# Optimization experiments

Hardware: AMD Instinct MI355X
Metric: run time of the kernel (lower is better)

Reference implementation:

```python
import jax, jax.numpy as jnp
import numpy as np

EPS = 1e-5

def _bn(x, g, b, m, v):
    # eval-mode batchnorm, NCHW, per-channel params
    inv = g / jnp.sqrt(v + EPS)
    return x * inv[None, :, None, None] + (b - m * inv)[None, :, None, None]

def setup_inputs() -> dict:
    key = jax.random.key(0)
    ks = jax.random.split(key, 16)
    C = 64
    x = jax.random.normal(ks[0], (8, C, 64, 64), dtype=jnp.float32)
    w1 = jax.random.normal(ks[1], (C, C, 1, 1), dtype=jnp.float32) * 0.1
    w2 = jax.random.normal(ks[2], (C, 1, 3, 3), dtype=jnp.float32) * 0.1
    w3 = jax.random.normal(ks[3], (C, C, 1, 1), dtype=jnp.float32) * 0.1
    def bn_params(k):
        k1, k2, k3, k4 = jax.random.split(k, 4)
        return (jax.random.uniform(k1, (C,)) + 0.5,
                jax.random.normal(k2, (C,)) * 0.1,
                jax.random.normal(k3, (C,)) * 0.1,
                jax.random.uniform(k4, (C,)) + 0.5)
    g1, b1, m1, v1 = bn_params(ks[4])
    g2, b2, m2, v2 = bn_params(ks[5])
    g3, b3, m3, v3 = bn_params(ks[6])
    return {"x": x, "w1": w1, "bn1_g": g1, "bn1_b": b1, "bn1_m": m1, "bn1_v": v1,
            "w2": w2, "bn2_g": g2, "bn2_b": b2, "bn2_m": m2, "bn2_v": v2,
            "w3": w3, "bn3_g": g3, "bn3_b": b3, "bn3_m": m3, "bn3_v": v3}

def reference(x, w1, bn1_g, bn1_b, bn1_m, bn1_v,
              w2, bn2_g, bn2_b, bn2_m, bn2_v,
              w3, bn3_g, bn3_b, bn3_m, bn3_v):
    B, c, h, w = x.shape
    N = h * w
    # conv1 (1x1) + BN + ReLU -> V
    v = jnp.einsum('bchw,oc->bohw', x, w1[:, :, 0, 0])
    v = jax.nn.relu(_bn(v, bn1_g, bn1_b, bn1_m, bn1_v))
    # attention over spatial positions: Q=K=x, single head, dim=c
    Q = x.reshape(B, c, N)          # bdn
    V = v.reshape(B, c, N)          # bdm
    scores = jnp.einsum('bdn,bdm->bnm', Q, Q) / (c ** 0.5)  # [B,N,N]
    prob = jax.nn.softmax(scores, axis=-1)
    out = jnp.einsum('bnm,bdm->bdn', prob, V).reshape(B, c, h, w)
    # depthwise conv + BN + ReLU
    out = jax.lax.conv_general_dilated(
        out, w2, window_strides=(1, 1), padding='SAME',
        dimension_numbers=('NCHW', 'OIHW', 'NCHW'), feature_group_count=c)
    out = jax.nn.relu(_bn(out, bn2_g, bn2_b, bn2_m, bn2_v))
    # pointwise conv + BN
    out = jnp.einsum('bchw,oc->bohw', out, w3[:, :, 0, 0])
    out = _bn(out, bn3_g, bn3_b, bn3_m, bn3_v)
    # residual (stride==1 and in_size==out_size)
    return out + x
```

## Files before the change

kernel.cpp:

```cpp
#include <hip/hip_runtime.h>
#include <stdint.h>

typedef __attribute__((ext_vector_type(8)))  short s16x8;
typedef __attribute__((ext_vector_type(16))) float f32x16;
typedef __attribute__((ext_vector_type(2)))  unsigned u32x2;

union CvtI4 { int4 i; s16x8 s; };
union CvtU4 { uint4 u; s16x8 s; };

__device__ __forceinline__ unsigned f2bf(float f) {
    union { float f; unsigned u; } v; v.f = f;
    return (v.u + 0x7fffu + ((v.u >> 16) & 1u)) >> 16;
}

__device__ __forceinline__ unsigned packbf(float lo, float hi) {
    union { float f; unsigned u; } a0, a1;
    a0.f = lo; a1.f = hi;
    return __builtin_amdgcn_perm(a1.u + 0x8000u, a0.u + 0x8000u, 0x07060302u);
}

__device__ __forceinline__ void gload_lds16(const unsigned short* gsrc, unsigned short* ldst) {
    __builtin_amdgcn_global_load_lds(
        (const __attribute__((address_space(1))) void*)gsrc,
        (__attribute__((address_space(3))) void*)ldst, 16, 0, 0);
}

__global__ __launch_bounds__(256) void k_prep(
    const float* __restrict__ x, const float* __restrict__ w1,
    const float* __restrict__ g1, const float* __restrict__ b1,
    const float* __restrict__ m1, const float* __restrict__ v1,
    unsigned short* __restrict__ xT, unsigned short* __restrict__ vbf)
{
    __shared__ float X[64 * 65];
    const int b    = blockIdx.x >> 7;
    const int n0   = ((blockIdx.x >> 1) & 63) << 6;
    const int half = blockIdx.x & 1;
    const int tid  = threadIdx.x;
    const float QS = 0.42466090014400953f;

    {
        const int r = tid >> 6, nn = tid & 63;
        const float* xb = x + (size_t)b * 262144 + n0 + nn;
#pragma unroll
        for (int cc = 0; cc < 16; ++cc) {
            int c = cc * 4 + r;
            X[c * 65 + nn] = xb[(size_t)c * 4096];
        }
    }
    __syncthreads();

    {
        const int n8 = tid >> 3, c8 = tid & 7;
        const int n = (half << 5) + n8;
        unsigned u[4];
#pragma unroll
        for (int j = 0; j < 4; ++j) {
            unsigned lo = f2bf(X[(c8 * 8 + 2 * j) * 65 + n] * QS);
            unsigned hi = f2bf(X[(c8 * 8 + 2 * j + 1) * 65 + n] * QS);
            u[j] = lo | (hi << 16);
        }
        uint4 pk; pk.x = u[0]; pk.y = u[1]; pk.z = u[2]; pk.w = u[3];
        *(uint4*)(xT + (((size_t)((b << 12) + n0 + n)) << 6) + (c8 << 3)) = pk;
    }

    {
        const int n = tid & 63, og = tid >> 6;
        float rX[64];
#pragma unroll
        for (int c = 0; c < 64; ++c) rX[c] = X[c * 65 + n];
        unsigned short* vb = vbf + (((size_t)(b << 6)) << 12) + n0 + n;
#pragma unroll 2
        for (int oo = 0; oo < 8; ++oo) {
            int o = (half << 5) + og * 8 + oo;
            float inv = g1[o] * rsqrtf(v1[o] + 1e-5f);
            float sh  = b1[o] - m1[o] * inv;
            float acc = 0.f;
#pragma unroll
            for (int c = 0; c < 64; ++c) acc = fmaf(w1[o * 64 + c], rX[c], acc);
            vb[(size_t)o << 12] = (unsigned short)f2bf(fmaxf(fmaf(acc, inv, sh), 0.f));
        }
    }
}

__global__ __launch_bounds__(1024, 4) void k_attn(
    const unsigned short* __restrict__ xT, const unsigned short* __restrict__ vbf,
    unsigned short* __restrict__ outO)
{
    __shared__ __align__(16) unsigned short Kl[2][2][64 * 64];
    __shared__ __align__(16) unsigned short Vl[2][2][64 * 64];
    __shared__ float rsL[16][32];
    __shared__ float dnm[128];

    const int b   = blockIdx.x & 7;
    const int qg2 = blockIdx.x >> 3;
    const int tid = threadIdx.x;
    const int w = tid >> 6, lane = tid & 63;
    const int l31 = lane & 31, half = lane >> 5;
    const int qbase = qg2 << 7;
    const int qd = w & 7, par = w >> 3;
    const int s  = qd & 1;
    const int t2 = qd >> 1;

    s16x8 Bq[4];
    {
        const unsigned short* qr = xT +
            (((size_t)((b << 12) + qbase + (t2 << 5) + l31)) << 6) + (half << 3);
#pragma unroll
        for (int kk = 0; kk < 4; ++kk) {
            CvtI4 c; c.i = *(const int4*)(qr + (kk << 4));
            Bq[kk] = c.s;
        }
    }

    const int pt    = w >> 3;
    const int sr    = ((w & 7) << 3) + (lane >> 3);
    const int swsc  = (lane & 7) ^ (lane >> 3);
    const unsigned short* kSrc = xT  + ((size_t)b << 18) + (sr << 6) + (swsc << 3);
    const unsigned short* vSrc = vbf + ((size_t)b << 18) + ((size_t)sr << 12) + (swsc << 3);
    const int ldsOff = (w & 7) << 9;

    gload_lds16(kSrc + ((size_t)pt << 12), &Kl[0][pt][0] + ldsOff);
    gload_lds16(vSrc + (pt << 6),          &Vl[0][pt][0] + ldsOff);
    __syncthreads();

    f32x16 O[2];
#pragma unroll
    for (int dl = 0; dl < 2; ++dl)
#pragma unroll
        for (int r = 0; r < 16; ++r) O[dl][r] = 0.f;
    float rs = 0.f;

    uint2 Gh[4];
    s16x8 Bvh[4];
    {
        const s16x8 z = {0, 0, 0, 0, 0, 0, 0, 0};
#pragma unroll
        for (int q = 0; q < 4; ++q) { Gh[q].x = 0u; Gh[q].y = 0u; }
#pragma unroll
        for (int j = 0; j < 4; ++j) Bvh[j] = z;
    }

    const int km = (s << 5) + l31;

    for (int p = 0; p < 32; ++p) {
        if (p < 31) {
            const int tn = ((p + 1) << 1) + pt;
            gload_lds16(kSrc + ((size_t)tn << 12), &Kl[(p + 1) & 1][pt][0] + ldsOff);
            gload_lds16(vSrc + (tn << 6),          &Vl[(p + 1) & 1][pt][0] + ldsOff);
        }

        const unsigned short* Kb = &Kl[p & 1][par][0];
        s16x8 Ak[4];
#pragma unroll
        for (int kk = 0; kk < 4; ++kk)
            Ak[kk] = *(const s16x8*)(Kb + (km << 6) + ((((kk << 1) + half) ^ (km & 7)) << 3));

        __builtin_amdgcn_s_setprio(1);
#pragma unroll
        for (int ksl = 0; ksl < 2; ++ksl) {
            u32x2 r0 = __builtin_amdgcn_permlane32_swap(Gh[2*ksl].x, Gh[2*ksl+1].x, false, false);
            u32x2 r1 = __builtin_amdgcn_permlane32_swap(Gh[2*ksl].y, Gh[2*ksl+1].y, false, false);
            CvtU4 ac;
            ac.u.x = r0.x; ac.u.y = r1.x; ac.u.z = r0.y; ac.u.w = r1.y;
            const s16x8 Ap = ac.s;
            O[0] = __builtin_amdgcn_mfma_f32_32x32x16_bf16(Ap, Bvh[0 + 2*ksl], O[0], 0, 0, 0);
            O[1] = __builtin_amdgcn_mfma_f32_32x32x16_bf16(Ap, Bvh[1 + 2*ksl], O[1], 0, 0, 0);
        }

        f32x16 S = {0.f,0.f,0.f,0.f,0.f,0.f,0.f,0.f,0.f,0.f,0.f,0.f,0.f,0.f,0.f,0.f};
        S = __builtin_amdgcn_mfma_f32_32x32x16_bf16(Ak[0], Bq[0], S, 0, 0, 0);
        S = __builtin_amdgcn_mfma_f32_32x32x16_bf16(Ak[1], Bq[1], S, 0, 0, 0);
        S = __builtin_amdgcn_mfma_f32_32x32x16_bf16(Ak[2], Bq[2], S, 0, 0, 0);
        S = __builtin_amdgcn_mfma_f32_32x32x16_bf16(Ak[3], Bq[3], S, 0, 0, 0);
        __builtin_amdgcn_s_setprio(0);

#pragma unroll
        for (int q = 0; q < 4; ++q) {
            float p0 = __builtin_amdgcn_exp2f(S[4*q+0]);
            float p1 = __builtin_amdgcn_exp2f(S[4*q+1]);
            float p2 = __builtin_amdgcn_exp2f(S[4*q+2]);
            float p3 = __builtin_amdgcn_exp2f(S[4*q+3]);
            rs += (p0 + p1) + (p2 + p3);
            Gh[q].x = packbf(p0, p1);
            Gh[q].y = packbf(p2, p3);
        }

        {
            const unsigned short* Vb = &Vl[p & 1][par][0];
#pragma unroll
            for (int ksl = 0; ksl < 2; ++ksl)
#pragma unroll
                for (int dl = 0; dl < 2; ++dl) {
                    const int drow = (dl << 5) + l31;
                    const int cch = (s << 2) + (ksl << 1) + half;
                    Bvh[2*ksl + dl] =
                        *(const s16x8*)(Vb + (drow << 6) + ((cch ^ (drow & 7)) << 3));
                }
        }

        __syncthreads();
    }

#pragma unroll
    for (int ksl = 0; ksl < 2; ++ksl) {
        u32x2 r0 = __builtin_amdgcn_permlane32_swap(Gh[2*ksl].x, Gh[2*ksl+1].x, false, false);
        u32x2 r1 = __builtin_amdgcn_permlane32_swap(Gh[2*ksl].y, Gh[2*ksl+1].y, false, false);
        CvtU4 ac;
        ac.u.x = r0.x; ac.u.y = r1.x; ac.u.z = r0.y; ac.u.w = r1.y;
        const s16x8 Ap = ac.s;
        O[0] = __builtin_amdgcn_mfma_f32_32x32x16_bf16(Ap, Bvh[0 + 2*ksl], O[0], 0, 0, 0);
        O[1] = __builtin_amdgcn_mfma_f32_32x32x16_bf16(Ap, Bvh[1 + 2*ksl], O[1], 0, 0, 0);
    }

    float* scrK = (float*)&Kl[0][0][0];
    float* scrV = (float*)&Vl[0][0][0];

    rs += __shfl_xor(rs, 32);
    if (half == 0) rsL[w][l31] = rs;

    if (par == 1) {
        float* rg = (qd < 4) ? (scrK + (qd << 11)) : (scrV + ((qd - 4) << 11));
#pragma unroll
        for (int dl = 0; dl < 2; ++dl)
#pragma unroll
            for (int r = 0; r < 16; ++r)
                rg[(dl << 10) + (r << 6) + lane] = O[dl][r];
    }
    __syncthreads();

    if (tid < 128) {
        int tt = tid >> 5, n32 = tid & 31;
        dnm[tid] = (rsL[(tt << 1) + 0][n32] + rsL[(tt << 1) + 1][n32]) +
                   (rsL[(tt << 1) + 8][n32] + rsL[(tt << 1) + 9][n32]);
    }
    if (par == 0) {
        float* rg = (qd < 4) ? (scrK + (qd << 11)) : (scrV + ((qd - 4) << 11));
#pragma unroll
        for (int dl = 0; dl < 2; ++dl)
#pragma unroll
            for (int r = 0; r < 16; ++r)
                O[dl][r] += rg[(dl << 10) + (r << 6) + lane];
    }
    __syncthreads();

    if (par == 0 && s == 1) {
#pragma unroll
        for (int dl = 0; dl < 2; ++dl)
#pragma unroll
            for (int r = 0; r < 16; ++r)
                scrK[(t2 << 11) + (dl << 10) + (r << 6) + lane] = O[dl][r];
    }
    __syncthreads();

    if (par == 0 && s == 0) {
        const int nb = (b << 12) + qbase;
#pragma unroll
        for (int dl = 0; dl < 2; ++dl)
#pragma unroll
            for (int r = 0; r < 16; ++r) {
                int rowoff = (r & 3) + ((r >> 2) << 3) + (half << 2);
                int n = (t2 << 5) + rowoff;
                float o = O[dl][r] + scrK[(t2 << 11) + (dl << 10) + (r << 6) + lane];
                outO[((size_t)(nb + n) << 6) + (dl << 5) + l31] =
                    (unsigned short)f2bf(o * (1.f / dnm[n]));
            }
    }
}

__global__ __launch_bounds__(256) void k_post(
    const unsigned short* __restrict__ Obase,
    const float* __restrict__ x,
    const float* __restrict__ w2,
    const float* __restrict__ g2, const float* __restrict__ b2,
    const float* __restrict__ m2, const float* __restrict__ v2,
    const float* __restrict__ w3,
    const float* __restrict__ g3, const float* __restrict__ b3,
    const float* __restrict__ m3, const float* __restrict__ v3,
    float* __restrict__ out)
{
    __shared__ float W[3][34 * 66];
    __shared__ float T2[32 * 66];

    const int b  = blockIdx.x >> 7;
    const int h  = (blockIdx.x >> 1) & 63;
    const int wh = blockIdx.x & 1;
    const int wbase = wh << 5;
    const int tid = threadIdx.x;

#pragma unroll
    for (int r = 0; r < 3; ++r) {
        int hh = h + r - 1;
#pragma unroll
        for (int i = 0; i < 2; ++i) {
            int lin = (i << 8) + tid;
            if (lin < 272) {
                int wl = lin >> 3, cg = lin & 7;
                int wg = wbase + wl - 1;
                float* Wd = &W[r][wl * 66 + (cg << 3)];
                if (hh >= 0 && hh <= 63 && wg >= 0 && wg <= 63) {
                    size_t npos = (size_t)((b << 12) + (hh << 6) + wg);
                    uint4 v = *(const uint4*)(Obase + (npos << 6) + (cg << 3));
                    union { float f; unsigned u; } t;
                    t.u = v.x << 16;         Wd[0] = t.f;
                    t.u = v.x & 0xFFFF0000u; Wd[1] = t.f;
                    t.u = v.y << 16;         Wd[2] = t.f;
                    t.u = v.y & 0xFFFF0000u; Wd[3] = t.f;
                    t.u = v.z << 16;         Wd[4] = t.f;
                    t.u = v.z & 0xFFFF0000u; Wd[5] = t.f;
                    t.u = v.w << 16;         Wd[6] = t.f;
                    t.u = v.w & 0xFFFF0000u; Wd[7] = t.f;
                } else {
#pragma unroll
                    for (int j = 0; j < 8; ++j) Wd[j] = 0.f;
                }
            }
        }
    }
    __syncthreads();

    const int w32 = tid & 31, cq = tid >> 5;
    float t8[8];
#pragma unroll
    for (int i = 0; i < 8; ++i) t8[i] = 0.f;

#pragma unroll
    for (int ky = 0; ky < 3; ++ky) {
#pragma unroll
        for (int kx = 0; kx < 3; ++kx) {
            const int k = ky * 3 + kx;
            const float* Wr = &W[ky][(w32 + kx) * 66 + (cq << 3)];
#pragma unroll
            for (int i = 0; i < 2; ++i) {
                float4 a = *(const float4*)(Wr + (i << 2));
                int c = (cq << 3) + (i << 2);
                t8[i * 4 + 0] = fmaf(w2[(c + 0) * 9 + k], a.x, t8[i * 4 + 0]);
                t8[i * 4 + 1] = fmaf(w2[(c + 1) * 9 + k], a.y, t8[i * 4 + 1]);
                t8[i * 4 + 2] = fmaf(w2[(c + 2) * 9 + k], a.z, t8[i * 4 + 2]);
                t8[i * 4 + 3] = fmaf(w2[(c + 3) * 9 + k], a.w, t8[i * 4 + 3]);
            }
        }
    }
#pragma unroll
    for (int i = 0; i < 8; ++i) {
        int c = (cq << 3) + i;
        float inv = g2[c] * rsqrtf(v2[c] + 1e-5f);
        float sh  = b2[c] - m2[c] * inv;
        T2[w32 * 66 + c] = fmaxf(fmaf(t8[i], inv, sh), 0.f);
    }
    __syncthreads();

    float rT[64];
#pragma unroll
    for (int c4 = 0; c4 < 16; ++c4)
        *(float4*)&rT[c4 << 2] = *(const float4*)&T2[w32 * 66 + (c4 << 2)];

    const int hw = (h << 6) + wbase + w32;
#pragma unroll 2
    for (int oo = 0; oo < 8; ++oo) {
        int o = (cq << 3) + oo;
        float inv = g3[o] * rsqrtf(v3[o] + 1e-5f);
        float sh  = b3[o] - m3[o] * inv;
        float acc = 0.f;
#pragma unroll
        for (int c = 0; c < 64; ++c) acc = fmaf(w3[o * 64 + c], rT[c], acc);
        size_t idx = (((size_t)((b << 6) + o)) << 12) + hw;
        out[idx] = fmaf(acc, inv, sh) + x[idx];
    }
}

extern "C" void kernel_launch(void* const* d_in, const int* in_sizes, int n_in,
                              void* d_out, int out_size, void* d_ws, size_t ws_size,
                              hipStream_t stream)
{
    const float* x  = (const float*)d_in[0];
    const float* w1 = (const float*)d_in[1];
    const float* g1 = (const float*)d_in[2];
    const float* b1 = (const float*)d_in[3];
    const float* m1 = (const float*)d_in[4];
    const float* v1 = (const float*)d_in[5];
    const float* w2 = (const float*)d_in[6];
    const float* g2 = (const float*)d_in[7];
    const float* b2 = (const float*)d_in[8];
    const float* m2 = (const float*)d_in[9];
    const float* v2 = (const float*)d_in[10];
    const float* w3 = (const float*)d_in[11];
    const float* g3 = (const float*)d_in[12];
    const float* b3 = (const float*)d_in[13];
    const float* m3 = (const float*)d_in[14];
    const float* v3 = (const float*)d_in[15];
    float* out = (float*)d_out;

    unsigned short* xT  = (unsigned short*)d_ws;
    unsigned short* vbf = xT + (size_t)8 * 4096 * 64;
    unsigned short* Obase = (unsigned short*)((char*)d_ws + (8u << 20));

    k_prep<<<1024, 256, 0, stream>>>(x, w1, g1, b1, m1, v1, xT, vbf);
    k_attn<<<256, 1024, 0, stream>>>(xT, vbf, Obase);
    k_post<<<1024, 256, 0, stream>>>(Obase, x, w2, g2, b2, m2, v2,
                                     w3, g3, b3, m3, v3, out);
}
```

Baseline: 183.7 us.

## Stage four key/value tiles per barrier in attention loop

The attention kernel now loads four 64-key K/V tiles per double-buffered stage instead of two, so each wave processes two tiles per iteration. This halves the number of loop iterations and __syncthreads barriers and issues more async global-to-LDS loads per wave at once. In exchange, K/V shared memory doubles, which may limit occupancy under the 1024-thread, 4-block launch bounds.

```diff
diff --git a/kernel.cpp b/kernel.cpp
--- a/kernel.cpp
+++ b/kernel.cpp
@@ -86,8 +86,8 @@
     const unsigned short* __restrict__ xT, const unsigned short* __restrict__ vbf,
     unsigned short* __restrict__ outO)
 {
-    __shared__ __align__(16) unsigned short Kl[2][2][64 * 64];
-    __shared__ __align__(16) unsigned short Vl[2][2][64 * 64];
+    __shared__ __align__(16) unsigned short Kl[2][4][64 * 64];
+    __shared__ __align__(16) unsigned short Vl[2][4][64 * 64];
     __shared__ float rsL[16][32];
     __shared__ float dnm[128];
 
@@ -112,15 +112,25 @@
         }
     }
 
-    const int pt    = w >> 3;
-    const int sr    = ((w & 7) << 3) + (lane >> 3);
-    const int swsc  = (lane & 7) ^ (lane >> 3);
-    const unsigned short* kSrc = xT  + ((size_t)b << 18) + (sr << 6) + (swsc << 3);
-    const unsigned short* vSrc = vbf + ((size_t)b << 18) + ((size_t)sr << 12) + (swsc << 3);
-    const int ldsOff = (w & 7) << 9;
-
-    gload_lds16(kSrc + ((size_t)pt << 12), &Kl[0][pt][0] + ldsOff);
-    gload_lds16(vSrc + (pt << 6),          &Vl[0][pt][0] + ldsOff);
+    int jt_[2], rg_[2];
+    {
+        int li0 = (w << 1), li1 = (w << 1) + 1;
+        jt_[0] = li0 >> 3; rg_[0] = li0 & 7;
+        jt_[1] = li1 >> 3; rg_[1] = li1 & 7;
+    }
+    const int lrow = lane >> 3;
+    const int swsc = (lane & 7) ^ lrow;
+    const unsigned short* kRow0 = xT  + ((size_t)b << 18) + (((rg_[0] << 3) + lrow) << 6) + (swsc << 3);
+    const unsigned short* kRow1 = xT  + ((size_t)b << 18) + (((rg_[1] << 3) + lrow) << 6) + (swsc << 3);
+    const unsigned short* vRow0 = vbf + ((size_t)b << 18) + ((size_t)((rg_[0] << 3) + lrow) << 12) + (swsc << 3);
+    const unsigned short* vRow1 = vbf + ((size_t)b << 18) + ((size_t)((rg_[1] << 3) + lrow) << 12) + (swsc << 3);
+    const int ldsOff0 = rg_[0] << 9;
+    const int ldsOff1 = rg_[1] << 9;
+
+    gload_lds16(kRow0 + ((size_t)jt_[0] << 12), &Kl[0][jt_[0]][0] + ldsOff0);
+    gload_lds16(kRow1 + ((size_t)jt_[1] << 12), &Kl[0][jt_[1]][0] + ldsOff1);
+    gload_lds16(vRow0 + (jt_[0] << 6),          &Vl[0][jt_[0]][0] + ldsOff0);
+    gload_lds16(vRow1 + (jt_[1] << 6),          &Vl[0][jt_[1]][0] + ldsOff1);
     __syncthreads();
 
     f32x16 O[2];
@@ -142,60 +152,68 @@
 
     const int km = (s << 5) + l31;
 
-    for (int p = 0; p < 32; ++p) {
-        if (p < 31) {
-            const int tn = ((p + 1) << 1) + pt;
-            gload_lds16(kSrc + ((size_t)tn << 12), &Kl[(p + 1) & 1][pt][0] + ldsOff);
-            gload_lds16(vSrc + (tn << 6),          &Vl[(p + 1) & 1][pt][0] + ldsOff);
-        }
-
-        const unsigned short* Kb = &Kl[p & 1][par][0];
-        s16x8 Ak[4];
-#pragma unroll
-        for (int kk = 0; kk < 4; ++kk)
-            Ak[kk] = *(const s16x8*)(Kb + (km << 6) + ((((kk << 1) + half) ^ (km & 7)) << 3));
-
-        __builtin_amdgcn_s_setprio(1);
-#pragma unroll
-        for (int ksl = 0; ksl < 2; ++ksl) {
-            u32x2 r0 = __builtin_amdgcn_permlane32_swap(Gh[2*ksl].x, Gh[2*ksl+1].x, false, false);
-            u32x2 r1 = __builtin_amdgcn_permlane32_swap(Gh[2*ksl].y, Gh[2*ksl+1].y, false, false);
-            CvtU4 ac;
-            ac.u.x = r0.x; ac.u.y = r1.x; ac.u.z = r0.y; ac.u.w = r1.y;
-            const s16x8 Ap = ac.s;
-            O[0] = __builtin_amdgcn_mfma_f32_32x32x16_bf16(Ap, Bvh[0 + 2*ksl], O[0], 0, 0, 0);
-            O[1] = __builtin_amdgcn_mfma_f32_32x32x16_bf16(Ap, Bvh[1 + 2*ksl], O[1], 0, 0, 0);
-        }
-
-        f32x16 S = {0.f,0.f,0.f,0.f,0.f,0.f,0.f,0.f,0.f,0.f,0.f,0.f,0.f,0.f,0.f,0.f};
-        S = __builtin_amdgcn_mfma_f32_32x32x16_bf16(Ak[0], Bq[0], S, 0, 0, 0);
-        S = __builtin_amdgcn_mfma_f32_32x32x16_bf16(Ak[1], Bq[1], S, 0, 0, 0);
-        S = __builtin_amdgcn_mfma_f32_32x32x16_bf16(Ak[2], Bq[2], S, 0, 0, 0);
-        S = __builtin_amdgcn_mfma_f32_32x32x16_bf16(Ak[3], Bq[3], S, 0, 0, 0);
-        __builtin_amdgcn_s_setprio(0);
-
-#pragma unroll
-        for (int q = 0; q < 4; ++q) {
-            float p0 = __builtin_amdgcn_exp2f(S[4*q+0]);
-            float p1 = __builtin_amdgcn_exp2f(S[4*q+1]);
-            float p2 = __builtin_amdgcn_exp2f(S[4*q+2]);
-            float p3 = __builtin_amdgcn_exp2f(S[4*q+3]);
-            rs += (p0 + p1) + (p2 + p3);
-            Gh[q].x = packbf(p0, p1);
-            Gh[q].y = packbf(p2, p3);
-        }
-
-        {
-            const unsigned short* Vb = &Vl[p & 1][par][0];
-#pragma unroll
-            for (int ksl = 0; ksl < 2; ++ksl)
-#pragma unroll
-                for (int dl = 0; dl < 2; ++dl) {
-                    const int drow = (dl << 5) + l31;
-                    const int cch = (s << 2) + (ksl << 1) + half;
-                    Bvh[2*ksl + dl] =
-                        *(const s16x8*)(Vb + (drow << 6) + ((cch ^ (drow & 7)) << 3));
-                }
+    for (int p = 0; p < 16; ++p) {
+        if (p < 15) {
+            const int t0 = ((p + 1) << 2) + jt_[0];
+            const int t1 = ((p + 1) << 2) + jt_[1];
+            gload_lds16(kRow0 + ((size_t)t0 << 12), &Kl[(p + 1) & 1][jt_[0]][0] + ldsOff0);
+            gload_lds16(kRow1 + ((size_t)t1 << 12), &Kl[(p + 1) & 1][jt_[1]][0] + ldsOff1);
+            gload_lds16(vRow0 + (t0 << 6),          &Vl[(p + 1) & 1][jt_[0]][0] + ldsOff0);
+            gload_lds16(vRow1 + (t1 << 6),          &Vl[(p + 1) & 1][jt_[1]][0] + ldsOff1);
+        }
+
+#pragma unroll
+        for (int jj = 0; jj < 2; ++jj) {
+            const int j = par + (jj << 1);
+
+            const unsigned short* Kb = &Kl[p & 1][j][0];
+            s16x8 Ak[4];
+#pragma unroll
+            for (int kk = 0; kk < 4; ++kk)
+                Ak[kk] = *(const s16x8*)(Kb + (km << 6) + ((((kk << 1) + half) ^ (km & 7)) << 3));
+
+            __builtin_amdgcn_s_setprio(1);
+#pragma unroll
+            for (int ksl = 0; ksl < 2; ++ksl) {
+                u32x2 r0 = __builtin_amdgcn_permlane32_swap(Gh[2*ksl].x, Gh[2*ksl+1].x, false, false);
+                u32x2 r1 = __builtin_amdgcn_permlane32_swap(Gh[2*ksl].y, Gh[2*ksl+1].y, false, false);
+                CvtU4 ac;
+                ac.u.x = r0.x; ac.u.y = r1.x; ac.u.z = r0.y; ac.u.w = r1.y;
+                const s16x8 Ap = ac.s;
+                O[0] = __builtin_amdgcn_mfma_f32_32x32x16_bf16(Ap, Bvh[0 + 2*ksl], O[0], 0, 0, 0);
+                O[1] = __builtin_amdgcn_mfma_f32_32x32x16_bf16(Ap, Bvh[1 + 2*ksl], O[1], 0, 0, 0);
+            }
+
+            f32x16 S = {0.f,0.f,0.f,0.f,0.f,0.f,0.f,0.f,0.f,0.f,0.f,0.f,0.f,0.f,0.f,0.f};
+            S = __builtin_amdgcn_mfma_f32_32x32x16_bf16(Ak[0], Bq[0], S, 0, 0, 0);
+            S = __builtin_amdgcn_mfma_f32_32x32x16_bf16(Ak[1], Bq[1], S, 0, 0, 0);
+            S = __builtin_amdgcn_mfma_f32_32x32x16_bf16(Ak[2], Bq[2], S, 0, 0, 0);
+            S = __builtin_amdgcn_mfma_f32_32x32x16_bf16(Ak[3], Bq[3], S, 0, 0, 0);
+            __builtin_amdgcn_s_setprio(0);
+
+#pragma unroll
+            for (int q = 0; q < 4; ++q) {
+                float p0 = __builtin_amdgcn_exp2f(S[4*q+0]);
+                float p1 = __builtin_amdgcn_exp2f(S[4*q+1]);
+                float p2 = __builtin_amdgcn_exp2f(S[4*q+2]);
+                float p3 = __builtin_amdgcn_exp2f(S[4*q+3]);
+                rs += (p0 + p1) + (p2 + p3);
+                Gh[q].x = packbf(p0, p1);
+                Gh[q].y = packbf(p2, p3);
+            }
+
+            {
+                const unsigned short* Vb = &Vl[p & 1][j][0];
+#pragma unroll
+                for (int ksl = 0; ksl < 2; ++ksl)
+#pragma unroll
+                    for (int dl = 0; dl < 2; ++dl) {
+                        const int drow = (dl << 5) + l31;
+                        const int cch = (s << 2) + (ksl << 1) + half;
+                        Bvh[2*ksl + dl] =
+                            *(const s16x8*)(Vb + (drow << 6) + ((cch ^ (drow & 7)) << 3));
+                    }
+            }
         }
 
         __syncthreads();
```

New measurement: 183.3 us. No clear change (-0.2%).

## Store K/V in MFMA fragment order and load directly to registers, dropping LDS staging

Applied to the files above, without the earlier changes.

The prep kernel now writes the scaled-x (K/Q) and V bf16 tensors pre-swizzled into the exact per-lane MFMA fragment layout, so each lane reads a contiguous 16-byte chunk. The attention kernel drops the double-buffered LDS staging with global_load_lds and the per-iteration __syncthreads, and loads K and V fragments straight from global memory into registers. The software pipelining that overlapped the previous tile's PV MFMAs with the current QK is also removed. Each wave now re-reads K/V from global or L2 with no cross-wave sharing through LDS, which puts load latency directly on the critical path and raises L2 traffic.

```diff
diff --git a/kernel.cpp b/kernel.cpp
--- a/kernel.cpp
+++ b/kernel.cpp
@@ -19,21 +19,16 @@
     return __builtin_amdgcn_perm(a1.u + 0x8000u, a0.u + 0x8000u, 0x07060302u);
 }
 
-__device__ __forceinline__ void gload_lds16(const unsigned short* gsrc, unsigned short* ldst) {
-    __builtin_amdgcn_global_load_lds(
-        (const __attribute__((address_space(1))) void*)gsrc,
-        (__attribute__((address_space(3))) void*)ldst, 16, 0, 0);
-}
-
 __global__ __launch_bounds__(256) void k_prep(
     const float* __restrict__ x, const float* __restrict__ w1,
     const float* __restrict__ g1, const float* __restrict__ b1,
     const float* __restrict__ m1, const float* __restrict__ v1,
-    unsigned short* __restrict__ xT, unsigned short* __restrict__ vbf)
+    unsigned short* __restrict__ xTf, unsigned short* __restrict__ vbff)
 {
     __shared__ float X[64 * 65];
     const int b    = blockIdx.x >> 7;
-    const int n0   = ((blockIdx.x >> 1) & 63) << 6;
+    const int n0g  = (blockIdx.x >> 1) & 63;
+    const int n0   = n0g << 6;
     const int half = blockIdx.x & 1;
     const int tid  = threadIdx.x;
     const float QS = 0.42466090014400953f;
@@ -51,16 +46,19 @@
 
     {
         const int n8 = tid >> 3, c8 = tid & 7;
-        const int n = (half << 5) + n8;
+        const int kk = c8 >> 1, hb = c8 & 1;
+        const int st = (n0g << 1) + half;
+        const int N  = (half << 5) + n8;
         unsigned u[4];
 #pragma unroll
         for (int j = 0; j < 4; ++j) {
-            unsigned lo = f2bf(X[(c8 * 8 + 2 * j) * 65 + n] * QS);
-            unsigned hi = f2bf(X[(c8 * 8 + 2 * j + 1) * 65 + n] * QS);
+            unsigned lo = f2bf(X[(c8 * 8 + 2 * j) * 65 + N] * QS);
+            unsigned hi = f2bf(X[(c8 * 8 + 2 * j + 1) * 65 + N] * QS);
             u[j] = lo | (hi << 16);
         }
         uint4 pk; pk.x = u[0]; pk.y = u[1]; pk.z = u[2]; pk.w = u[3];
-        *(uint4*)(xT + (((size_t)((b << 12) + n0 + n)) << 6) + (c8 << 3)) = pk;
+        *(uint4*)(xTf + ((((size_t)((b << 7) + st) << 2) + kk) << 9)
+                      + ((n8 + (hb << 5)) << 3)) = pk;
     }
 
     {
@@ -68,7 +66,10 @@
         float rX[64];
 #pragma unroll
         for (int c = 0; c < 64; ++c) rX[c] = X[c * 65 + n];
-        unsigned short* vb = vbf + (((size_t)(b << 6)) << 12) + n0 + n;
+        const int cn = n >> 3, e = n & 7;
+        const int sS = cn >> 2, kslS = (cn >> 1) & 1, hb = cn & 1;
+        unsigned short* vb = vbff +
+            ((((size_t)((b << 6) + n0g) << 3) + (sS << 2) + (kslS << 1) + half) << 9) + e;
 #pragma unroll 2
         for (int oo = 0; oo < 8; ++oo) {
             int o = (half << 5) + og * 8 + oo;
@@ -77,17 +78,17 @@
             float acc = 0.f;
 #pragma unroll
             for (int c = 0; c < 64; ++c) acc = fmaf(w1[o * 64 + c], rX[c], acc);
-            vb[(size_t)o << 12] = (unsigned short)f2bf(fmaxf(fmaf(acc, inv, sh), 0.f));
+            int lane = (og * 8 + oo) + (hb << 5);
+            vb[lane << 3] = (unsigned short)f2bf(fmaxf(fmaf(acc, inv, sh), 0.f));
         }
     }
 }
 
 __global__ __launch_bounds__(1024, 4) void k_attn(
-    const unsigned short* __restrict__ xT, const unsigned short* __restrict__ vbf,
+    const unsigned short* __restrict__ xTf, const unsigned short* __restrict__ vbff,
     unsigned short* __restrict__ outO)
 {
-    __shared__ __align__(16) unsigned short Kl[2][2][64 * 64];
-    __shared__ __align__(16) unsigned short Vl[2][2][64 * 64];
+    __shared__ float scr[16384];
     __shared__ float rsL[16][32];
     __shared__ float dnm[128];
 
@@ -103,25 +104,17 @@
 
     s16x8 Bq[4];
     {
-        const unsigned short* qr = xT +
-            (((size_t)((b << 12) + qbase + (t2 << 5) + l31)) << 6) + (half << 3);
+        const unsigned short* qB = xTf +
+            (((size_t)((b << 7) + (qg2 << 2) + t2)) << 11) + (lane << 3);
 #pragma unroll
         for (int kk = 0; kk < 4; ++kk) {
-            CvtI4 c; c.i = *(const int4*)(qr + (kk << 4));
+            CvtI4 c; c.i = *(const int4*)(qB + (kk << 9));
             Bq[kk] = c.s;
         }
     }
 
-    const int pt    = w >> 3;
-    const int sr    = ((w & 7) << 3) + (lane >> 3);
-    const int swsc  = (lane & 7) ^ (lane >> 3);
-    const unsigned short* kSrc = xT  + ((size_t)b << 18) + (sr << 6) + (swsc << 3);
-    const unsigned short* vSrc = vbf + ((size_t)b << 18) + ((size_t)sr << 12) + (swsc << 3);
-    const int ldsOff = (w & 7) << 9;
-
-    gload_lds16(kSrc + ((size_t)pt << 12), &Kl[0][pt][0] + ldsOff);
-    gload_lds16(vSrc + (pt << 6),          &Vl[0][pt][0] + ldsOff);
-    __syncthreads();
+    const unsigned short* akB = xTf  + (((size_t)((b << 9) + (s << 2))) << 9) + (lane << 3);
+    const unsigned short* bvB = vbff + (((size_t)((b << 9) + (s << 2))) << 9) + (lane << 3);
 
     f32x16 O[2];
 #pragma unroll
@@ -130,50 +123,26 @@
         for (int r = 0; r < 16; ++r) O[dl][r] = 0.f;
     float rs = 0.f;
 
-    uint2 Gh[4];
-    s16x8 Bvh[4];
-    {
-        const s16x8 z = {0, 0, 0, 0, 0, 0, 0, 0};
-#pragma unroll
-        for (int q = 0; q < 4; ++q) { Gh[q].x = 0u; Gh[q].y = 0u; }
-#pragma unroll
-        for (int j = 0; j < 4; ++j) Bvh[j] = z;
-    }
-
-    const int km = (s << 5) + l31;
-
-    for (int p = 0; p < 32; ++p) {
-        if (p < 31) {
-            const int tn = ((p + 1) << 1) + pt;
-            gload_lds16(kSrc + ((size_t)tn << 12), &Kl[(p + 1) & 1][pt][0] + ldsOff);
-            gload_lds16(vSrc + (tn << 6),          &Vl[(p + 1) & 1][pt][0] + ldsOff);
-        }
-
-        const unsigned short* Kb = &Kl[p & 1][par][0];
-        s16x8 Ak[4];
-#pragma unroll
-        for (int kk = 0; kk < 4; ++kk)
-            Ak[kk] = *(const s16x8*)(Kb + (km << 6) + ((((kk << 1) + half) ^ (km & 7)) << 3));
-
+    for (int it = 0; it < 32; ++it) {
+        const size_t toff = ((size_t)((it << 1) + par)) << 12;
+
+        int4 ar[4], br[4];
+#pragma unroll
+        for (int kk = 0; kk < 4; ++kk) ar[kk] = *(const int4*)(akB + (kk << 9) + toff);
+#pragma unroll
+        for (int j = 0; j < 4; ++j)    br[j]  = *(const int4*)(bvB + (j << 9) + toff);
+
+        f32x16 S = {0.f,0.f,0.f,0.f,0.f,0.f,0.f,0.f,0.f,0.f,0.f,0.f,0.f,0.f,0.f,0.f};
         __builtin_amdgcn_s_setprio(1);
-#pragma unroll
-        for (int ksl = 0; ksl < 2; ++ksl) {
-            u32x2 r0 = __builtin_amdgcn_permlane32_swap(Gh[2*ksl].x, Gh[2*ksl+1].x, false, false);
-            u32x2 r1 = __builtin_amdgcn_permlane32_swap(Gh[2*ksl].y, Gh[2*ksl+1].y, false, false);
-            CvtU4 ac;
-            ac.u.x = r0.x; ac.u.y = r1.x; ac.u.z = r0.y; ac.u.w = r1.y;
-            const s16x8 Ap = ac.s;
-            O[0] = __builtin_amdgcn_mfma_f32_32x32x16_bf16(Ap, Bvh[0 + 2*ksl], O[0], 0, 0, 0);
-            O[1] = __builtin_amdgcn_mfma_f32_32x32x16_bf16(Ap, Bvh[1 + 2*ksl], O[1], 0, 0, 0);
-        }
-
-        f32x16 S = {0.f,0.f,0.f,0.f,0.f,0.f,0.f,0.f,0.f,0.f,0.f,0.f,0.f,0.f,0.f,0.f};
-        S = __builtin_amdgcn_mfma_f32_32x32x16_bf16(Ak[0], Bq[0], S, 0, 0, 0);
-        S = __builtin_amdgcn_mfma_f32_32x32x16_bf16(Ak[1], Bq[1], S, 0, 0, 0);
-        S = __builtin_amdgcn_mfma_f32_32x32x16_bf16(Ak[2], Bq[2], S, 0, 0, 0);
-        S = __builtin_amdgcn_mfma_f32_32x32x16_bf16(Ak[3], Bq[3], S, 0, 0, 0);
+        {
+            CvtI4 c0; c0.i = ar[0]; S = __builtin_amdgcn_mfma_f32_32x32x16_bf16(c0.s, Bq[0], S, 0, 0, 0);
+            CvtI4 c1; c1.i = ar[1]; S = __builtin_amdgcn_mfma_f32_32x32x16_bf16(c1.s, Bq[1], S, 0, 0, 0);
+            CvtI4 c2; c2.i = ar[2]; S = __builtin_amdgcn_mfma_f32_32x32x16_bf16(c2.s, Bq[2], S, 0, 0, 0);
+            CvtI4 c3; c3.i = ar[3]; S = __builtin_amdgcn_mfma_f32_32x32x16_bf16(c3.s, Bq[3], S, 0, 0, 0);
+        }
         __builtin_amdgcn_s_setprio(0);
 
+        uint2 G[4];
 #pragma unroll
         for (int q = 0; q < 4; ++q) {
             float p0 = __builtin_amdgcn_exp2f(S[4*q+0]);
@@ -181,39 +150,28 @@
             float p2 = __builtin_amdgcn_exp2f(S[4*q+2]);
             float p3 = __builtin_amdgcn_exp2f(S[4*q+3]);
             rs += (p0 + p1) + (p2 + p3);
-            Gh[q].x = packbf(p0, p1);
-            Gh[q].y = packbf(p2, p3);
-        }
-
-        {
-            const unsigned short* Vb = &Vl[p & 1][par][0];
-#pragma unroll
-            for (int ksl = 0; ksl < 2; ++ksl)
-#pragma unroll
-                for (int dl = 0; dl < 2; ++dl) {
-                    const int drow = (dl << 5) + l31;
-                    const int cch = (s << 2) + (ksl << 1) + half;
-                    Bvh[2*ksl + dl] =
-                        *(const s16x8*)(Vb + (drow << 6) + ((cch ^ (drow & 7)) << 3));
-                }
-        }
-
-        __syncthreads();
-    }
-
-#pragma unroll
-    for (int ksl = 0; ksl < 2; ++ksl) {
-        u32x2 r0 = __builtin_amdgcn_permlane32_swap(Gh[2*ksl].x, Gh[2*ksl+1].x, false, false);
-        u32x2 r1 = __builtin_amdgcn_permlane32_swap(Gh[2*ksl].y, Gh[2*ksl+1].y, false, false);
-        CvtU4 ac;
-        ac.u.x = r0.x; ac.u.y = r1.x; ac.u.z = r0.y; ac.u.w = r1.y;
-        const s16x8 Ap = ac.s;
-        O[0] = __builtin_amdgcn_mfma_f32_32x32x16_bf16(Ap, Bvh[0 + 2*ksl], O[0], 0, 0, 0);
-        O[1] = __builtin_amdgcn_mfma_f32_32x32x16_bf16(Ap, Bvh[1 + 2*ksl], O[1], 0, 0, 0);
-    }
-
-    float* scrK = (float*)&Kl[0][0][0];
-    float* scrV = (float*)&Vl[0][0][0];
+            G[q].x = packbf(p0, p1);
+            G[q].y = packbf(p2, p3);
+        }
+
+        __builtin_amdgcn_s_setprio(1);
+#pragma unroll
+        for (int ksl = 0; ksl < 2; ++ksl) {
+            u32x2 r0 = __builtin_amdgcn_permlane32_swap(G[2*ksl].x, G[2*ksl+1].x, false, false);
+            u32x2 r1 = __builtin_amdgcn_permlane32_swap(G[2*ksl].y, G[2*ksl+1].y, false, false);
+            CvtU4 ac;
+            ac.u.x = r0.x; ac.u.y = r1.x; ac.u.z = r0.y; ac.u.w = r1.y;
+            const s16x8 Ap = ac.s;
+            CvtI4 v0; v0.i = br[2*ksl + 0];
+            CvtI4 v1; v1.i = br[2*ksl + 1];
+            O[0] = __builtin_amdgcn_mfma_f32_32x32x16_bf16(Ap, v0.s, O[0], 0, 0, 0);
+            O[1] = __builtin_amdgcn_mfma_f32_32x32x16_bf16(Ap, v1.s, O[1], 0, 0, 0);
+        }
+        __builtin_amdgcn_s_setprio(0);
+    }
+
+    float* scrK = scr;
+    float* scrV = scr + 8192;
 
     rs += __shfl_xor(rs, 32);
     if (half == 0) rsL[w][l31] = rs;
@@ -390,12 +348,12 @@
     const float* v3 = (const float*)d_in[15];
     float* out = (float*)d_out;
 
-    unsigned short* xT  = (unsigned short*)d_ws;
-    unsigned short* vbf = xT + (size_t)8 * 4096 * 64;
+    unsigned short* xTf  = (unsigned short*)d_ws;
+    unsigned short* vbff = xTf + (size_t)8 * 4096 * 64;
     unsigned short* Obase = (unsigned short*)((char*)d_ws + (8u << 20));
 
-    k_prep<<<1024, 256, 0, stream>>>(x, w1, g1, b1, m1, v1, xT, vbf);
-    k_attn<<<256, 1024, 0, stream>>>(xT, vbf, Obase);
+    k_prep<<<1024, 256, 0, stream>>>(x, w1, g1, b1, m1, v1, xTf, vbff);
+    k_attn<<<256, 1024, 0, stream>>>(xTf, vbff, Obase);
     k_post<<<1024, 256, 0, stream>>>(Obase, x, w2, g2, b2, m2, v2,
                                      w3, g3, b3, m3, v3, out);
 }
```

Measured after the change: 180.9 us, median of 2. Within noise of the previous version (-1.5%).
